# Optimization experiments

Measured on AMD Instinct MI355X. Metric: run time of the kernel, lower is better.

The kernel has to match this reference:

```python
import jax, jax.numpy as jnp
import numpy as np

K, T, D, S, A, C, H = 128, 64, 128, 512, 4, 16, 512
N_LEAVES = 128
TEMP = 1.0          # sample_merge_temp
EPS_SQRT = 1e-4     # distances.EPSILON ** 0.5 with EPSILON = 1e-8
_SQ_EPS = 1e-12     # numerical guard inside sqrt (diagonal of pairwise dists is 0)


def setup_inputs() -> dict:
    key = jax.random.key(0)
    ks = jax.random.split(key, 11)
    leaf_counts_Kxt = jax.random.randint(ks[0], (K, T), 1, 5)
    embeddings_KxtxD = jax.random.normal(ks[1], (K, T, D), jnp.float32)
    log_felsensteins_KxtxSxA = jax.random.normal(ks[2], (K, T, S, A), jnp.float32)
    site_positions_SxC = jax.random.uniform(ks[3], (S, C), jnp.float32)
    W1 = jax.random.normal(ks[4], (2 * D, H), jnp.float32) / jnp.sqrt(2.0 * D)
    b1 = jnp.zeros((H,), jnp.float32)
    W2 = jax.random.normal(ks[5], (H, D), jnp.float32) / jnp.sqrt(1.0 * H)
    b2 = jnp.zeros((D,), jnp.float32)
    gumbel_Kxtt = jax.random.gumbel(ks[6], (K, T * T), jnp.float32)
    u1_K = jax.random.uniform(ks[7], (K,), jnp.float32, minval=1e-6, maxval=1.0)
    u2_K = jax.random.uniform(ks[8], (K,), jnp.float32, minval=1e-6, maxval=1.0)
    return {
        "N": N_LEAVES,
        "leaf_counts_Kxt": leaf_counts_Kxt,
        "embeddings_KxtxD": embeddings_KxtxD,
        "log_felsensteins_KxtxSxA": log_felsensteins_KxtxSxA,
        "site_positions_SxC": site_positions_SxC,
        "W1": W1, "b1": b1, "W2": W2, "b2": b2,
        "gumbel_Kxtt": gumbel_Kxtt, "u1_K": u1_K, "u2_K": u2_K,
    }


def _merge_encoder(c1_KxD, c2_KxD, W1, b1, W2, b2):
    # MLP merge encoder: MLP(concat(child1, child2)) -> parent embedding
    h = jax.nn.relu(jnp.concatenate([c1_KxD, c2_KxD], axis=-1) @ W1 + b1)
    return h @ W2 + b2


def reference(N, leaf_counts_Kxt, embeddings_KxtxD, log_felsensteins_KxtxSxA,
              site_positions_SxC, W1, b1, W2, b2, gumbel_Kxtt, u1_K, u2_K):
    Kp, t = leaf_counts_Kxt.shape
    ar = jnp.arange(Kp)

    # --- pairwise distances over all t*t subtree pairs per particle ---
    diff_Kxtxtxd = embeddings_KxtxD[:, :, None, :] - embeddings_KxtxD[:, None, :, :]
    pd_Kxtxt = jnp.sqrt(jnp.sum(diff_Kxtxtxd * diff_Kxtxtxd, axis=-1) + _SQ_EPS)
    merge_log_weights_Kxtxt = -pd_Kxtxt / TEMP
    # diagonal_scatter(-inf): forbid self-merges
    eye = jnp.eye(t, dtype=bool)[None]
    merge_log_weights_Kxtxt = jnp.where(eye, -jnp.inf, merge_log_weights_Kxtxt)

    # --- categorical merge sampling (gumbel-max with pre-drawn noise) ---
    flat_Kxtt = merge_log_weights_Kxtxt.reshape(Kp, t * t)
    sample_K = jnp.argmax(flat_Kxtt + gumbel_Kxtt, axis=1)
    idx1_K = sample_K // t
    idx2_K = sample_K % t
    log_merge_prob_K = (flat_Kxtt[ar, sample_K] + jnp.log(2.0)
                        - jax.scipy.special.logsumexp(flat_Kxtt, axis=1))

    # --- merged embedding ---
    child1_KxD = embeddings_KxtxD[ar, idx1_K]
    child2_KxD = embeddings_KxtxD[ar, idx2_K]
    embedding_KxD = _merge_encoder(child1_KxD, child2_KxD, W1, b1, W2, b2)

    # --- branch lengths sampled from Exp(rate = 1/(dist + eps)) ---
    d1_K = jnp.sqrt(jnp.sum((child1_KxD - embedding_KxD) ** 2, axis=-1) + _SQ_EPS)
    d2_K = jnp.sqrt(jnp.sum((child2_KxD - embedding_KxD) ** 2, axis=-1) + _SQ_EPS)
    rate1_K = 1.0 / (d1_K + EPS_SQRT)
    rate2_K = 1.0 / (d2_K + EPS_SQRT)
    branch1_K = -(1.0 / rate1_K) * jnp.log(u1_K)
    branch2_K = -(1.0 / rate2_K) * jnp.log(u2_K)
    log_branch1_prior_K = jnp.log(rate1_K) - rate1_K * branch1_K
    log_branch2_prior_K = jnp.log(rate2_K) - rate2_K * branch2_K

    log_v_plus_K = log_merge_prob_K + log_branch1_prior_K + log_branch2_prior_K

    # --- over-counting correction ---
    ones_K = jnp.sum(leaf_counts_Kxt == 1, axis=1)
    ones_K = ones_K - (leaf_counts_Kxt[ar, idx1_K] == 1).astype(ones_K.dtype)
    ones_K = ones_K - (leaf_counts_Kxt[ar, idx2_K] == 1).astype(ones_K.dtype)
    log_v_minus_K = jnp.log((N - ones_K).astype(jnp.float32))

    return (idx1_K, idx2_K, branch1_K, branch2_K, embedding_KxD,
            log_v_plus_K, log_v_minus_K)
```

## Files before the change

### kernel.cpp

```cpp
#include <hip/hip_runtime.h>
#include <math.h>

#define Kp 128
#define Tn 64
#define Dn 128
#define Hn 512
#define ETS 68

__global__ __launch_bounds__(256, 1) void ep_kernel(
    const int*   __restrict__ Nptr,
    const int*   __restrict__ leaf,
    const float* __restrict__ emb,
    const float* __restrict__ W1,
    const float* __restrict__ b1,
    const float* __restrict__ W2,
    const float* __restrict__ b2,
    const float* __restrict__ gum,
    const float* __restrict__ u1,
    const float* __restrict__ u2,
    float* __restrict__ out)
{
    const int k    = blockIdx.x;
    const int tid  = threadIdx.x;
    const int lane = tid & 63;
    const int wid  = tid >> 6;

    __shared__ float ET[Dn * ETS];
    __shared__ float xs[256];
    __shared__ float hsh[Hn];
    __shared__ float part[256];
    __shared__ float nI[Tn];
    __shared__ float sBest[4]; __shared__ int sIdx[4]; __shared__ float sW[4]; __shared__ float sM[4];
    __shared__ float sSum[4];
    __shared__ float sD1[4]; __shared__ float sD2[4];
    __shared__ int   sOnes;
    __shared__ int   fIdx; __shared__ float fW; __shared__ float fM;
    __shared__ float embs[Dn];

    if (tid < 64) {
        int lc = leaf[k * Tn + tid];
        unsigned long long m = __ballot(lc == 1);
        if (tid == 0) sOnes = __popcll(m);
    }

    {
        const float4* src = (const float4*)(emb + (size_t)k * Tn * Dn);
        #pragma unroll
        for (int it = 0; it < 8; ++it) {
            int f4 = tid + it * 256;
            float4 v = src[f4];
            int e0 = f4 * 4;
            int i = e0 >> 7;
            int d = e0 & 127;
            ET[(d + 0) * ETS + i] = v.x;
            ET[(d + 1) * ETS + i] = v.y;
            ET[(d + 2) * ETS + i] = v.z;
            ET[(d + 3) * ETS + i] = v.w;
        }
    }
    __syncthreads();

    const int tx = tid & 15;
    const int ty = tid >> 4;
    float acc[4][4] = {};
    #pragma unroll 4
    for (int d = 0; d < Dn; ++d) {
        float4 a = *(const float4*)&ET[d * ETS + 4 * ty];
        float4 b = *(const float4*)&ET[d * ETS + 4 * tx];
        float ar[4] = {a.x, a.y, a.z, a.w};
        float br[4] = {b.x, b.y, b.z, b.w};
        #pragma unroll
        for (int r = 0; r < 4; ++r)
            #pragma unroll
            for (int c = 0; c < 4; ++c)
                acc[r][c] += ar[r] * br[c];
    }
    if (tx == ty) {
        #pragma unroll
        for (int c = 0; c < 4; ++c) nI[4 * tx + c] = acc[c][c];
    }
    __syncthreads();

    float wreg[16];
    float maxw = -INFINITY;
    float best = -INFINITY, bestW = 0.0f;
    int   bestIdx = 0;
    {
        const float* gk = gum + (size_t)k * (Tn * Tn);
        #pragma unroll
        for (int r = 0; r < 4; ++r) {
            int i = 4 * ty + r;
            float4 g4 = *(const float4*)&gk[i * Tn + 4 * tx];
            float gv[4] = {g4.x, g4.y, g4.z, g4.w};
            float ni = nI[i];
            #pragma unroll
            for (int c = 0; c < 4; ++c) {
                int j = 4 * tx + c;
                float pd2 = ni + nI[j] - 2.0f * acc[r][c];
                pd2 = fmaxf(pd2, 0.0f) + 1e-12f;
                float wv = (i == j) ? -INFINITY : -sqrtf(pd2);
                wreg[r * 4 + c] = wv;
                maxw = fmaxf(maxw, wv);
                float wg = wv + gv[c];
                int idx = i * Tn + j;
                if (wg > best || (wg == best && idx < bestIdx)) {
                    best = wg; bestIdx = idx; bestW = wv;
                }
            }
        }
    }

    #pragma unroll
    for (int off = 32; off > 0; off >>= 1) {
        float ob = __shfl_down(best, off);
        int   oi = __shfl_down(bestIdx, off);
        float ow = __shfl_down(bestW, off);
        float om = __shfl_down(maxw, off);
        if (ob > best || (ob == best && oi < bestIdx)) { best = ob; bestIdx = oi; bestW = ow; }
        maxw = fmaxf(maxw, om);
    }
    if (lane == 0) { sBest[wid] = best; sIdx[wid] = bestIdx; sW[wid] = bestW; sM[wid] = maxw; }
    __syncthreads();
    if (tid == 0) {
        best = sBest[0]; bestIdx = sIdx[0]; bestW = sW[0]; maxw = sM[0];
        #pragma unroll
        for (int q = 1; q < 4; ++q) {
            if (sBest[q] > best || (sBest[q] == best && sIdx[q] < bestIdx)) {
                best = sBest[q]; bestIdx = sIdx[q]; bestW = sW[q];
            }
            maxw = fmaxf(maxw, sM[q]);
        }
        fIdx = bestIdx; fW = bestW; fM = maxw;
    }
    __syncthreads();

    const int   i1 = fIdx >> 6;
    const int   i2 = fIdx & 63;
    const float M  = fM;

    float es = 0.0f;
    #pragma unroll
    for (int q = 0; q < 16; ++q) es += expf(wreg[q] - M);
    #pragma unroll
    for (int off = 32; off > 0; off >>= 1) es += __shfl_down(es, off);
    if (lane == 0) sSum[wid] = es;

    xs[tid] = (tid < 128) ? ET[tid * ETS + i1] : ET[(tid - 128) * ETS + i2];
    __syncthreads();

    {
        const int j0 = 2 * tid;
        float a0 = b1[j0], a1 = b1[j0 + 1];
        #pragma unroll 4
        for (int i = 0; i < 256; i += 4) {
            float4 x  = *(const float4*)&xs[i];
            float2 w0 = *(const float2*)&W1[(i + 0) * Hn + j0];
            float2 w1 = *(const float2*)&W1[(i + 1) * Hn + j0];
            float2 w2 = *(const float2*)&W1[(i + 2) * Hn + j0];
            float2 w3 = *(const float2*)&W1[(i + 3) * Hn + j0];
            a0 += x.x * w0.x; a1 += x.x * w0.y;
            a0 += x.y * w1.x; a1 += x.y * w1.y;
            a0 += x.z * w2.x; a1 += x.z * w2.y;
            a0 += x.w * w3.x; a1 += x.w * w3.y;
        }
        hsh[j0]     = fmaxf(a0, 0.0f);
        hsh[j0 + 1] = fmaxf(a1, 0.0f);
    }
    __syncthreads();

    {
        const int dd = tid & 127;
        const int hh = tid >> 7;
        float ac = 0.0f;
        const int jbase = hh * 256;
        #pragma unroll 4
        for (int j = jbase; j < jbase + 256; j += 4) {
            float4 hv = *(const float4*)&hsh[j];
            ac += hv.x * W2[(j + 0) * Dn + dd];
            ac += hv.y * W2[(j + 1) * Dn + dd];
            ac += hv.z * W2[(j + 2) * Dn + dd];
            ac += hv.w * W2[(j + 3) * Dn + dd];
        }
        part[tid] = ac;
    }
    __syncthreads();
    if (tid < 128) {
        float e = part[tid] + part[tid + 128] + b2[tid];
        embs[tid] = e;
        out[4 * Kp + k * Dn + tid] = e;
    }
    __syncthreads();

    float v1 = 0.0f, v2 = 0.0f;
    if (tid < 128) {
        float e  = embs[tid];
        float q1 = xs[tid] - e;        v1 = q1 * q1;
        float q2 = xs[128 + tid] - e;  v2 = q2 * q2;
    }
    #pragma unroll
    for (int off = 32; off > 0; off >>= 1) {
        v1 += __shfl_down(v1, off);
        v2 += __shfl_down(v2, off);
    }
    if (lane == 0) { sD1[wid] = v1; sD2[wid] = v2; }
    __syncthreads();

    if (tid == 0) {
        float s1 = sD1[0] + sD1[1] + sD1[2] + sD1[3];
        float s2 = sD2[0] + sD2[1] + sD2[2] + sD2[3];
        float d1 = sqrtf(s1 + 1e-12f);
        float d2 = sqrtf(s2 + 1e-12f);
        float rate1 = 1.0f / (d1 + 1e-4f);
        float rate2 = 1.0f / (d2 + 1e-4f);
        float u1v = u1[k], u2v = u2[k];
        float branch1 = -(1.0f / rate1) * logf(u1v);
        float branch2 = -(1.0f / rate2) * logf(u2v);
        float lbp1 = logf(rate1) - rate1 * branch1;
        float lbp2 = logf(rate2) - rate2 * branch2;
        float ssum = sSum[0] + sSum[1] + sSum[2] + sSum[3];
        float lse  = fM + logf(ssum);
        float lmp  = fW + 0.69314718055994531f - lse;
        float lvp  = lmp + lbp1 + lbp2;
        int lc1 = leaf[k * Tn + i1];
        int lc2 = leaf[k * Tn + i2];
        int ones = sOnes - (lc1 == 1 ? 1 : 0) - (lc2 == 1 ? 1 : 0);
        float lvm = logf((float)(Nptr[0] - ones));

        out[k]                       = (float)i1;
        out[Kp + k]                  = (float)i2;
        out[2 * Kp + k]              = branch1;
        out[3 * Kp + k]              = branch2;
        out[4 * Kp + Kp * Dn + k]      = lvp;
        out[4 * Kp + Kp * Dn + Kp + k] = lvm;
    }
}

extern "C" void kernel_launch(void* const* d_in, const int* in_sizes, int n_in,
                              void* d_out, int out_size, void* d_ws, size_t ws_size,
                              hipStream_t stream) {
    const int*   Nptr = (const int*)  d_in[0];
    const int*   leaf = (const int*)  d_in[1];
    const float* emb  = (const float*)d_in[2];
    const float* W1   = (const float*)d_in[5];
    const float* b1   = (const float*)d_in[6];
    const float* W2   = (const float*)d_in[7];
    const float* b2   = (const float*)d_in[8];
    const float* gum  = (const float*)d_in[9];
    const float* u1   = (const float*)d_in[10];
    const float* u2   = (const float*)d_in[11];
    float* out = (float*)d_out;

    ep_kernel<<<Kp, 256, 0, stream>>>(Nptr, leaf, emb, W1, b1, W2, b2, gum, u1, u2, out);
}
```

Before: 136.7 us.

## Prefetch inputs early, drop max-shift in softmax, split MLP reductions across threads

Embedding and Gumbel loads are issued into registers before the shared-memory transpose, so their latency overlaps. The log-sum-exp no longer subtracts the max, because all weights are at most zero, which removes one reduction round and a barrier. Both MLP layers now use float4 weight loads, with the input dimension split across thread groups and partial sums reduced in shared memory. The cost is extra registers and a few more barriers, plus a small numerical risk from the unshifted exp sum.

```diff
diff --git a/kernel.cpp b/kernel.cpp
--- a/kernel.cpp
+++ b/kernel.cpp
@@ -28,13 +28,13 @@
     __shared__ float ET[Dn * ETS];
     __shared__ float xs[256];
     __shared__ float hsh[Hn];
-    __shared__ float part[256];
+    __shared__ float buf[1024];
     __shared__ float nI[Tn];
-    __shared__ float sBest[4]; __shared__ int sIdx[4]; __shared__ float sW[4]; __shared__ float sM[4];
+    __shared__ float sBest[4]; __shared__ int sIdx[4]; __shared__ float sW[4];
     __shared__ float sSum[4];
     __shared__ float sD1[4]; __shared__ float sD2[4];
     __shared__ int   sOnes;
-    __shared__ int   fIdx; __shared__ float fW; __shared__ float fM;
+    __shared__ int   fIdx; __shared__ float fW;
     __shared__ float embs[Dn];
 
     if (tid < 64) {
@@ -43,25 +43,34 @@
         if (tid == 0) sOnes = __popcll(m);
     }
 
-    {
-        const float4* src = (const float4*)(emb + (size_t)k * Tn * Dn);
-        #pragma unroll
-        for (int it = 0; it < 8; ++it) {
-            int f4 = tid + it * 256;
-            float4 v = src[f4];
-            int e0 = f4 * 4;
-            int i = e0 >> 7;
-            int d = e0 & 127;
-            ET[(d + 0) * ETS + i] = v.x;
-            ET[(d + 1) * ETS + i] = v.y;
-            ET[(d + 2) * ETS + i] = v.z;
-            ET[(d + 3) * ETS + i] = v.w;
-        }
-    }
-    __syncthreads();
-
     const int tx = tid & 15;
     const int ty = tid >> 4;
+    float4 ev[8];
+    {
+        const float4* src = (const float4*)(emb + (size_t)k * Tn * Dn);
+        #pragma unroll
+        for (int it = 0; it < 8; ++it) ev[it] = src[tid + it * 256];
+    }
+    float4 g4[4];
+    {
+        const float* gk = gum + (size_t)k * (Tn * Tn);
+        #pragma unroll
+        for (int r = 0; r < 4; ++r) g4[r] = *(const float4*)&gk[(4 * ty + r) * Tn + 4 * tx];
+    }
+
+    #pragma unroll
+    for (int it = 0; it < 8; ++it) {
+        int f4 = tid + it * 256;
+        int e0 = f4 * 4;
+        int i = e0 >> 7;
+        int d = e0 & 127;
+        ET[(d + 0) * ETS + i] = ev[it].x;
+        ET[(d + 1) * ETS + i] = ev[it].y;
+        ET[(d + 2) * ETS + i] = ev[it].z;
+        ET[(d + 3) * ETS + i] = ev[it].w;
+    }
+    __syncthreads();
+
     float acc[4][4] = {};
     #pragma unroll 4
     for (int d = 0; d < Dn; ++d) {
@@ -81,31 +90,25 @@
     }
     __syncthreads();
 
-    float wreg[16];
-    float maxw = -INFINITY;
+    float es = 0.0f;
     float best = -INFINITY, bestW = 0.0f;
     int   bestIdx = 0;
-    {
-        const float* gk = gum + (size_t)k * (Tn * Tn);
-        #pragma unroll
-        for (int r = 0; r < 4; ++r) {
-            int i = 4 * ty + r;
-            float4 g4 = *(const float4*)&gk[i * Tn + 4 * tx];
-            float gv[4] = {g4.x, g4.y, g4.z, g4.w};
-            float ni = nI[i];
-            #pragma unroll
-            for (int c = 0; c < 4; ++c) {
-                int j = 4 * tx + c;
-                float pd2 = ni + nI[j] - 2.0f * acc[r][c];
-                pd2 = fmaxf(pd2, 0.0f) + 1e-12f;
-                float wv = (i == j) ? -INFINITY : -sqrtf(pd2);
-                wreg[r * 4 + c] = wv;
-                maxw = fmaxf(maxw, wv);
-                float wg = wv + gv[c];
-                int idx = i * Tn + j;
-                if (wg > best || (wg == best && idx < bestIdx)) {
-                    best = wg; bestIdx = idx; bestW = wv;
-                }
+    #pragma unroll
+    for (int r = 0; r < 4; ++r) {
+        int i = 4 * ty + r;
+        float ni = nI[i];
+        float gv[4] = {g4[r].x, g4[r].y, g4[r].z, g4[r].w};
+        #pragma unroll
+        for (int c = 0; c < 4; ++c) {
+            int j = 4 * tx + c;
+            float pd2 = ni + nI[j] - 2.0f * acc[r][c];
+            pd2 = fmaxf(pd2, 0.0f) + 1e-12f;
+            float wv = (i == j) ? -INFINITY : -sqrtf(pd2);
+            es += expf(wv);
+            float wg = wv + gv[c];
+            int idx = i * Tn + j;
+            if (wg > best || (wg == best && idx < bestIdx)) {
+                best = wg; bestIdx = idx; bestW = wv;
             }
         }
     }
@@ -115,77 +118,83 @@
         float ob = __shfl_down(best, off);
         int   oi = __shfl_down(bestIdx, off);
         float ow = __shfl_down(bestW, off);
-        float om = __shfl_down(maxw, off);
+        float oe = __shfl_down(es, off);
         if (ob > best || (ob == best && oi < bestIdx)) { best = ob; bestIdx = oi; bestW = ow; }
-        maxw = fmaxf(maxw, om);
-    }
-    if (lane == 0) { sBest[wid] = best; sIdx[wid] = bestIdx; sW[wid] = bestW; sM[wid] = maxw; }
+        es += oe;
+    }
+    if (lane == 0) { sBest[wid] = best; sIdx[wid] = bestIdx; sW[wid] = bestW; sSum[wid] = es; }
     __syncthreads();
     if (tid == 0) {
-        best = sBest[0]; bestIdx = sIdx[0]; bestW = sW[0]; maxw = sM[0];
+        best = sBest[0]; bestIdx = sIdx[0]; bestW = sW[0];
         #pragma unroll
         for (int q = 1; q < 4; ++q) {
             if (sBest[q] > best || (sBest[q] == best && sIdx[q] < bestIdx)) {
                 best = sBest[q]; bestIdx = sIdx[q]; bestW = sW[q];
             }
-            maxw = fmaxf(maxw, sM[q]);
-        }
-        fIdx = bestIdx; fW = bestW; fM = maxw;
-    }
-    __syncthreads();
-
-    const int   i1 = fIdx >> 6;
-    const int   i2 = fIdx & 63;
-    const float M  = fM;
-
-    float es = 0.0f;
-    #pragma unroll
-    for (int q = 0; q < 16; ++q) es += expf(wreg[q] - M);
-    #pragma unroll
-    for (int off = 32; off > 0; off >>= 1) es += __shfl_down(es, off);
-    if (lane == 0) sSum[wid] = es;
+        }
+        fIdx = bestIdx; fW = bestW;
+    }
+    __syncthreads();
+
+    const int i1 = fIdx >> 6;
+    const int i2 = fIdx & 63;
 
     xs[tid] = (tid < 128) ? ET[tid * ETS + i1] : ET[(tid - 128) * ETS + i2];
     __syncthreads();
 
     {
-        const int j0 = 2 * tid;
-        float a0 = b1[j0], a1 = b1[j0 + 1];
+        const int j0 = 4 * (tid & 127);
+        const int ih = tid >> 7;
+        const float* W1r = W1 + j0;
+        float a0 = 0.0f, a1 = 0.0f, a2 = 0.0f, a3 = 0.0f;
+        const int ibase = ih * 128;
         #pragma unroll 4
-        for (int i = 0; i < 256; i += 4) {
+        for (int i = ibase; i < ibase + 128; i += 4) {
             float4 x  = *(const float4*)&xs[i];
-            float2 w0 = *(const float2*)&W1[(i + 0) * Hn + j0];
-            float2 w1 = *(const float2*)&W1[(i + 1) * Hn + j0];
-            float2 w2 = *(const float2*)&W1[(i + 2) * Hn + j0];
-            float2 w3 = *(const float2*)&W1[(i + 3) * Hn + j0];
-            a0 += x.x * w0.x; a1 += x.x * w0.y;
-            a0 += x.y * w1.x; a1 += x.y * w1.y;
-            a0 += x.z * w2.x; a1 += x.z * w2.y;
-            a0 += x.w * w3.x; a1 += x.w * w3.y;
-        }
-        hsh[j0]     = fmaxf(a0, 0.0f);
-        hsh[j0 + 1] = fmaxf(a1, 0.0f);
-    }
-    __syncthreads();
-
-    {
-        const int dd = tid & 127;
-        const int hh = tid >> 7;
-        float ac = 0.0f;
-        const int jbase = hh * 256;
+            float4 w0 = *(const float4*)&W1r[(size_t)(i + 0) * Hn];
+            float4 w1 = *(const float4*)&W1r[(size_t)(i + 1) * Hn];
+            float4 w2 = *(const float4*)&W1r[(size_t)(i + 2) * Hn];
+            float4 w3 = *(const float4*)&W1r[(size_t)(i + 3) * Hn];
+            a0 += x.x * w0.x + x.y * w1.x + x.z * w2.x + x.w * w3.x;
+            a1 += x.x * w0.y + x.y * w1.y + x.z * w2.y + x.w * w3.y;
+            a2 += x.x * w0.z + x.y * w1.z + x.z * w2.z + x.w * w3.z;
+            a3 += x.x * w0.w + x.y * w1.w + x.z * w2.w + x.w * w3.w;
+        }
+        *(float4*)&buf[ih * Hn + j0] = make_float4(a0, a1, a2, a3);
+    }
+    __syncthreads();
+    {
+        int j = tid;
+        hsh[j] = fmaxf(buf[j] + buf[Hn + j] + b1[j], 0.0f);
+        j = tid + 256;
+        hsh[j] = fmaxf(buf[j] + buf[Hn + j] + b1[j], 0.0f);
+    }
+    __syncthreads();
+
+    {
+        const int jh  = tid >> 5;
+        const int dd4 = 4 * (tid & 31);
+        float a0 = 0.0f, a1 = 0.0f, a2 = 0.0f, a3 = 0.0f;
+        const int jbase = jh * 64;
         #pragma unroll 4
-        for (int j = jbase; j < jbase + 256; j += 4) {
-            float4 hv = *(const float4*)&hsh[j];
-            ac += hv.x * W2[(j + 0) * Dn + dd];
-            ac += hv.y * W2[(j + 1) * Dn + dd];
-            ac += hv.z * W2[(j + 2) * Dn + dd];
-            ac += hv.w * W2[(j + 3) * Dn + dd];
-        }
-        part[tid] = ac;
+        for (int j = jbase; j < jbase + 64; j += 4) {
+            float4 h4 = *(const float4*)&hsh[j];
+            float4 w0 = *(const float4*)&W2[(size_t)(j + 0) * Dn + dd4];
+            float4 w1 = *(const float4*)&W2[(size_t)(j + 1) * Dn + dd4];
+            float4 w2 = *(const float4*)&W2[(size_t)(j + 2) * Dn + dd4];
+            float4 w3 = *(const float4*)&W2[(size_t)(j + 3) * Dn + dd4];
+            a0 += h4.x * w0.x + h4.y * w1.x + h4.z * w2.x + h4.w * w3.x;
+            a1 += h4.x * w0.y + h4.y * w1.y + h4.z * w2.y + h4.w * w3.y;
+            a2 += h4.x * w0.z + h4.y * w1.z + h4.z * w2.z + h4.w * w3.z;
+            a3 += h4.x * w0.w + h4.y * w1.w + h4.z * w2.w + h4.w * w3.w;
+        }
+        *(float4*)&buf[jh * Dn + dd4] = make_float4(a0, a1, a2, a3);
     }
     __syncthreads();
     if (tid < 128) {
-        float e = part[tid] + part[tid + 128] + b2[tid];
+        float e = b2[tid];
+        #pragma unroll
+        for (int q = 0; q < 8; ++q) e += buf[q * Dn + tid];
         embs[tid] = e;
         out[4 * Kp + k * Dn + tid] = e;
     }
@@ -218,7 +227,7 @@
         float lbp1 = logf(rate1) - rate1 * branch1;
         float lbp2 = logf(rate2) - rate2 * branch2;
         float ssum = sSum[0] + sSum[1] + sSum[2] + sSum[3];
-        float lse  = fM + logf(ssum);
+        float lse  = logf(ssum);
         float lmp  = fW + 0.69314718055994531f - lse;
         float lvp  = lmp + lbp1 + lbp2;
         int lc1 = leaf[k * Tn + i1];
```

New measurement: 131.2 us. -4.0%, faster.
